# Kernel optimization log

Hardware: AMD Instinct MI355X
Metric: run time of the kernel (lower is better)

Reference implementation:

```python
import jax, jax.numpy as jnp
import numpy as np

N = 100000          # nodes
E = 1600000         # edges
NS_IN = 128         # input scalars (128x0e)
MUL_IN = 32         # input 1o multiplicity -> eq dim 96
NS_OUT = 64         # output scalars (64x0e)
MUL_OUT = 16        # output 1o multiplicity -> eq dim 48
HID = 256           # ScalarMLPFunction hidden width
WNUM = MUL_IN * MUL_OUT  # o3.Linear weight_numel (single l=1 path)


def setup_inputs() -> dict:
    key = jax.random.key(0)
    ks = jax.random.split(key, 6)
    return {
        "features": jax.random.normal(ks[0], (N, NS_IN + MUL_IN * 3), jnp.float32),
        "edge_index": jax.random.randint(ks[1], (2, E), 0, N, dtype=jnp.int32),
        "inv_W1": jax.random.normal(ks[2], (NS_IN, HID), jnp.float32),
        "inv_W2": jax.random.normal(ks[3], (HID, NS_OUT), jnp.float32),
        "wemb_W1": jax.random.normal(ks[4], (NS_IN, HID), jnp.float32),
        "wemb_W2": jax.random.normal(ks[5], (HID, WNUM), jnp.float32),
    }


def _mlp(x, W1, W2):
    # ScalarMLPFunction: fan-in-normalized linears with SiLU nonlinearity
    h = jax.nn.silu((x @ W1) * np.float32(1.0 / np.sqrt(W1.shape[0])))
    return (h @ W2) * np.float32(1.0 / np.sqrt(W2.shape[0]))


def reference(features, edge_index, inv_W1, inv_W2, wemb_W1, wemb_W2):
    # active_nodes = torch.unique(edge_index[0]); expressed jit-compatibly as a
    # boolean mask (out_features starts at zero; only active rows are written).
    active = jnp.zeros((N,), jnp.bool_).at[edge_index[0]].set(True)

    scalars = features[:, :NS_IN]                       # [N, 128]

    # invariant readout MLP -> first n_scalars_out channels
    inv_out = _mlp(scalars, inv_W1, inv_W2)             # [N, 64]

    # equivariant path: reshape_in -> [N, mul_in, 3]
    x_eq = features[:, NS_IN:].reshape(N, MUL_IN, 3)
    # per-node o3.Linear weights from weights_emb MLP
    w = _mlp(scalars, wemb_W1, wemb_W2).reshape(N, MUL_IN, MUL_OUT)
    # e3nn o3.Linear (shared_weights=False), single l=1 path, path-normalized
    eq_out = jnp.einsum('nim,nio->nom', x_eq, w) * np.float32(1.0 / np.sqrt(MUL_IN))
    eq_flat = eq_out.reshape(N, MUL_OUT * 3)            # inverse_reshape_irreps

    out = jnp.concatenate([inv_out, eq_flat], axis=-1)  # [N, 112]
    return out * active[:, None].astype(out.dtype)
```

## Files before the change

kernel.cpp:

```cpp
#include <hip/hip_runtime.h>

#define NN 100000
#define EE 1600000
#define FDIM 224
#define OUTC 112

#define SPO 0
#define HCG 16384
#define RNG 32768
#define XO  32768
#define WMO 65536
#define LDSZ 81920

typedef __attribute__((ext_vector_type(8))) short bf16x8;
typedef __attribute__((ext_vector_type(4))) float f32x4;
typedef __attribute__((ext_vector_type(4))) unsigned int u32x4;
typedef __attribute__((ext_vector_type(4))) int i32x4;

__device__ __forceinline__ unsigned short f2bf(float f) {
  unsigned u = __builtin_bit_cast(unsigned, f);
  u = (u + 0x7FFFu + ((u >> 16) & 1u)) >> 16;
  return (unsigned short)u;
}
__device__ __forceinline__ float bf2f(unsigned short h) {
  return __builtin_bit_cast(float, (unsigned)h << 16);
}
__device__ __forceinline__ unsigned cvtpk(float lo, float hi) {
  unsigned d;
  asm("v_cvt_pk_bf16_f32 %0, %1, %2" : "=v"(d) : "v"(lo), "v"(hi));
  return d;
}
__device__ __forceinline__ float fast_exp2(float t) {
  float e; asm("v_exp_f32 %0, %1" : "=v"(e) : "v"(t)); return e;
}
__device__ __forceinline__ float fast_rcp(float x) {
  float r; asm("v_rcp_f32 %0, %1" : "=v"(r) : "v"(x)); return r;
}
__device__ __forceinline__ float silu_rs(float a) {
  float v = a * 0.08838834764831845f;
  float e = fast_exp2(v * -1.442695041f);
  return v * fast_rcp(1.f + e);
}
__device__ __forceinline__ void gl_lds16(const unsigned short* g, char* l) {
  __builtin_amdgcn_global_load_lds(
      (const __attribute__((address_space(1))) unsigned int*)g,
      (__attribute__((address_space(3))) unsigned int*)l, 16, 0, 0);
}

#define WAITV(n) do { asm volatile("s_waitcnt vmcnt(" #n ")" ::: "memory"); \
                      __builtin_amdgcn_sched_barrier(0); } while (0)
#define WAITV_FOR(c) do { if ((c) <= 52) { WAITV(3); } else if ((c) == 53) { WAITV(2); } \
                          else if ((c) == 54) { WAITV(1); } else { WAITV(0); } } while (0)
#define LGKM0() asm volatile("s_waitcnt lgkmcnt(0)" ::: "memory")
#define LGKM_BAR() do { asm volatile("s_waitcnt lgkmcnt(0)" ::: "memory"); \
                        __builtin_amdgcn_s_barrier(); } while (0)
#define KEEP(x) asm volatile("" :: "v"(x))
#define MFMA(A, B, C) __builtin_amdgcn_mfma_f32_16x16x32_bf16((A), (B), (C), 0, 0, 0)
#define ISSUE(c) do { if ((c) < 56) \
    gl_lds16(Wall + (size_t)(c) * 4096 + wv * 512 + lane * 8, \
             smem + RNG + ((c) & 3) * 8192 + wv * 1024); } while (0)

__global__ void k_zero(unsigned int* p, int n) {
  int i = blockIdx.x * 256 + threadIdx.x;
  if (i < n) p[i] = 0u;
}

__global__ void k_scatter(const int* __restrict__ ei, unsigned char* __restrict__ act) {
  int e4 = blockIdx.x * 256 + threadIdx.x;
  if (e4 < EE / 4) {
    i32x4 v = *(const i32x4*)(ei + e4 * 4);
#pragma unroll
    for (int j = 0; j < 4; ++j) {
      int n = v[j];
      if (!act[n]) act[n] = 1;
    }
  }
}

__global__ void k_wprep(const float* __restrict__ invW1, const float* __restrict__ invW2,
                        const float* __restrict__ wembW1, const float* __restrict__ wembW2,
                        unsigned short* __restrict__ Wall) {
  int i = blockIdx.x * 256 + threadIdx.x;
  if (i >= 56 * 4096) return;
  int c = i >> 12, j = i & 4095;
  float v;
  if (c < 16) {
    int cg = c >> 3, sub = c & 7;
    if (sub < 4) {
      int r128 = j >> 5, slot = (j >> 3) & 3, e = j & 7;
      int gg = slot ^ (r128 & 3);
      int hc = cg * 128 + r128;
      int k = sub * 32 + gg * 8 + e;
      v = (hc < 256) ? invW1[k * 256 + hc] : wembW1[k * 256 + (hc - 256)];
    } else {
      int ks = sub - 4;
      int wseg = j >> 9, r16 = (j >> 5) & 15, slot = (j >> 3) & 3, e = j & 7;
      int gg = slot ^ (r16 & 3);
      int col = (wseg >> 1) * 16 + r16;
      int k = cg * 128 + ks * 32 + gg * 8 + e;
      v = invW2[k * 64 + col];
    }
  } else {
    int c2 = c - 16;
    int cgl = c2 / 20, sub = c2 % 20;
    int r128 = j >> 5, slot = (j >> 3) & 3, e = j & 7;
    int gg = slot ^ (r128 & 3);
    if (sub < 4) {
      int hc = (2 + cgl) * 128 + r128;
      int k = sub * 32 + gg * 8 + e;
      v = (hc < 256) ? invW1[k * 256 + hc] : wembW1[k * 256 + (hc - 256)];
    } else {
      int idx = sub - 4, ct = idx >> 2, ks = idx & 3;
      int col = ct * 128 + r128;
      int k = cgl * 128 + ks * 32 + gg * 8 + e;
      v = wembW2[k * 512 + col];
    }
  }
  Wall[i] = f2bf(v);
}

__global__ __launch_bounds__(512, 2) void k_main(
    const float* __restrict__ feats,
    const unsigned short* __restrict__ Wall,
    const unsigned char* __restrict__ act,
    float* __restrict__ out) {
  __shared__ char smem[LDSZ];
  const int tid = threadIdx.x;
  const int lane = tid & 63;
  const int wv = tid >> 6;
  const int o = lane & 15;
  const int g = lane >> 4;
  const int base = blockIdx.x * 64;

  const float inv16 = 0.0625f;
  const float rs32  = 0.17677669529663687f;

  const int srow = tid >> 3, sq = tid & 7;
  int gnode = base + srow; if (gnode > NN - 1) gnode = NN - 1;
  const float* sp = feats + (size_t)gnode * FDIM + sq * 16;
  f32x4 s0 = *(const f32x4*)sp;
  f32x4 s1 = *(const f32x4*)(sp + 4);
  f32x4 s2 = *(const f32x4*)(sp + 8);
  f32x4 s3 = *(const f32x4*)(sp + 12);
  const float* xp = feats + (size_t)gnode * FDIM + 128 + sq * 12;
  f32x4 x0 = *(const f32x4*)xp;
  f32x4 x1 = *(const f32x4*)(xp + 4);
  f32x4 x2 = *(const f32x4*)(xp + 8);

  {
    unsigned w0 = cvtpk(s0[0], s0[1]), w1 = cvtpk(s0[2], s0[3]);
    unsigned w2 = cvtpk(s1[0], s1[1]), w3 = cvtpk(s1[2], s1[3]);
    unsigned w4 = cvtpk(s2[0], s2[1]), w5 = cvtpk(s2[2], s2[3]);
    unsigned w6 = cvtpk(s3[0], s3[1]), w7 = cvtpk(s3[2], s3[3]);
    *(u32x4*)(smem + SPO + srow * 256 + (((sq * 2 + 0) ^ (srow & 15)) << 4)) =
        (u32x4){w0, w1, w2, w3};
    *(u32x4*)(smem + SPO + srow * 256 + (((sq * 2 + 1) ^ (srow & 15)) << 4)) =
        (u32x4){w4, w5, w6, w7};
  }
  unsigned xr[6];
  xr[0] = cvtpk(x0[0], x0[1]); xr[1] = cvtpk(x0[2], x0[3]);
  xr[2] = cvtpk(x1[0], x1[1]); xr[3] = cvtpk(x1[2], x1[3]);
  xr[4] = cvtpk(x2[0], x2[1]); xr[5] = cvtpk(x2[2], x2[3]);
#pragma unroll
  for (int j = 0; j < 6; ++j) KEEP(xr[j]);
  asm volatile("s_waitcnt vmcnt(0)" ::: "memory");
  LGKM_BAR();

  ISSUE(0); ISSUE(1); ISSUE(2); ISSUE(3);

  f32x4 accW[4][4], accA[4], acc2[2];
#pragma unroll
  for (int ct = 0; ct < 4; ++ct)
#pragma unroll
    for (int rt = 0; rt < 4; ++rt) accW[ct][rt] = (f32x4){0.f, 0.f, 0.f, 0.f};
#pragma unroll
  for (int rt = 0; rt < 4; ++rt) accA[rt] = (f32x4){0.f, 0.f, 0.f, 0.f};
  acc2[0] = (f32x4){0.f, 0.f, 0.f, 0.f};
  acc2[1] = (f32x4){0.f, 0.f, 0.f, 0.f};

#pragma unroll
  for (int cg = 0; cg < 4; ++cg) {
    const int cb = (cg < 2) ? cg * 8 : 16 + (cg - 2) * 20;
#pragma unroll
    for (int ks = 0; ks < 4; ++ks) {
      const int c = cb + ks;
      WAITV_FOR(c);
      __builtin_amdgcn_s_setprio(1);
      bf16x8 b = *(const bf16x8*)(smem + RNG + (c & 3) * 8192 +
                                  (wv * 16 + o) * 64 + ((g ^ (o & 3)) << 4));
#pragma unroll
      for (int rt = 0; rt < 4; ++rt) {
        bf16x8 a = *(const bf16x8*)(smem + SPO + (rt * 16 + o) * 256 +
                                    (((ks * 4 + g) ^ o) << 4));
        accA[rt] = MFMA(a, b, accA[rt]);
      }
      __builtin_amdgcn_s_setprio(0);
      LGKM0();
      ISSUE(c + 4);
    }
    {
      const int col = wv * 16 + o;
#pragma unroll
      for (int rt = 0; rt < 4; ++rt) {
#pragma unroll
        for (int rp = 0; rp < 2; ++rp) {
          unsigned w = cvtpk(silu_rs(accA[rt][rp * 2]), silu_rs(accA[rt][rp * 2 + 1]));
          int row0 = rt * 16 + g * 4 + rp * 2;
          *(unsigned short*)(smem + HCG + row0 * 256 +
                             ((col * 2) ^ ((row0 & 15) << 4))) = (unsigned short)w;
          int row1 = row0 + 1;
          *(unsigned short*)(smem + HCG + row1 * 256 +
                             ((col * 2) ^ ((row1 & 15) << 4))) = (unsigned short)(w >> 16);
        }
        accA[rt] = (f32x4){0.f, 0.f, 0.f, 0.f};
      }
    }
    LGKM_BAR();
    if (cg < 2) {
#pragma unroll
      for (int ks = 0; ks < 4; ++ks) {
        const int c = cb + 4 + ks;
        WAITV_FOR(c);
        __builtin_amdgcn_s_setprio(1);
        bf16x8 b = *(const bf16x8*)(smem + RNG + (c & 3) * 8192 + wv * 1024 +
                                    o * 64 + ((g ^ (o & 3)) << 4));
        const int rtl = wv & 1;
        bf16x8 a0 = *(const bf16x8*)(smem + HCG + (rtl * 16 + o) * 256 +
                                     (((ks * 4 + g) ^ o) << 4));
        bf16x8 a1 = *(const bf16x8*)(smem + HCG + ((rtl + 2) * 16 + o) * 256 +
                                     (((ks * 4 + g) ^ o) << 4));
        acc2[0] = MFMA(a0, b, acc2[0]);
        acc2[1] = MFMA(a1, b, acc2[1]);
        __builtin_amdgcn_s_setprio(0);
        LGKM0();
        ISSUE(c + 4);
      }
    } else {
#pragma unroll
      for (int ct = 0; ct < 4; ++ct)
#pragma unroll
        for (int ks = 0; ks < 4; ++ks) {
          const int c = cb + 4 + ct * 4 + ks;
          WAITV_FOR(c);
          __builtin_amdgcn_s_setprio(1);
          bf16x8 b = *(const bf16x8*)(smem + RNG + (c & 3) * 8192 +
                                      (wv * 16 + o) * 64 + ((g ^ (o & 3)) << 4));
#pragma unroll
          for (int rt = 0; rt < 4; ++rt) {
            bf16x8 a = *(const bf16x8*)(smem + HCG + (rt * 16 + o) * 256 +
                                        (((ks * 4 + g) ^ o) << 4));
            accW[ct][rt] = MFMA(a, b, accW[ct][rt]);
          }
          __builtin_amdgcn_s_setprio(0);
          LGKM0();
          ISSUE(c + 4);
        }
    }
    LGKM_BAR();
  }

  {
    const int xb = XO + srow * 192 + sq * 24;
#pragma unroll
    for (int j = 0; j < 6; ++j) *(unsigned*)(smem + xb + j * 4) = xr[j];
  }
  float eq[6] = {0.f, 0.f, 0.f, 0.f, 0.f, 0.f};
  const int nloc = tid >> 3, q = tid & 7;
#pragma unroll
  for (int Q = 0; Q < 4; ++Q) {
    const int lc = wv * 16 + o;
#pragma unroll
    for (int rt = 0; rt < 4; ++rt)
#pragma unroll
      for (int rp = 0; rp < 2; ++rp) {
        unsigned w = cvtpk(accW[Q][rt][rp * 2] * inv16, accW[Q][rt][rp * 2 + 1] * inv16);
        int n0 = rt * 16 + g * 4 + rp * 2;
        *(unsigned short*)(smem + WMO + n0 * 256 +
                           ((lc * 2) ^ ((n0 & 15) << 4))) = (unsigned short)w;
        int n1 = n0 + 1;
        *(unsigned short*)(smem + WMO + n1 * 256 +
                           ((lc * 2) ^ ((n1 & 15) << 4))) = (unsigned short)(w >> 16);
      }
    LGKM_BAR();
#pragma unroll
    for (int il = 0; il < 8; ++il) {
      unsigned wpair = *(const unsigned*)(smem + WMO + nloc * 256 +
                                          ((il * 32 + q * 4) ^ ((nloc & 15) << 4)));
      float wf0 = bf2f((unsigned short)wpair);
      float wf1 = bf2f((unsigned short)(wpair >> 16));
      const int xb = XO + nloc * 192 + (Q * 24 + il * 3) * 2;
#pragma unroll
      for (int m = 0; m < 3; ++m) {
        float xv = bf2f(*(const unsigned short*)(smem + xb + m * 2));
        eq[m] += xv * wf0;
        eq[3 + m] += xv * wf1;
      }
    }
    if (Q < 3) LGKM_BAR();
  }

#pragma unroll
  for (int jj = 0; jj < 2; ++jj) {
    const int rt = (wv & 1) + jj * 2;
#pragma unroll
    for (int r = 0; r < 4; ++r) {
      int node = base + rt * 16 + g * 4 + r;
      if (node < NN) {
        float s = act[node] ? inv16 : 0.f;
        out[(size_t)node * OUTC + (wv >> 1) * 16 + o] = acc2[jj][r] * s;
      }
    }
  }
  {
    int node = base + nloc;
    if (node < NN) {
      float sC = act[node] ? rs32 : 0.f;
      float* op = out + (size_t)node * OUTC + 64 + q * 6;
#pragma unroll
      for (int j = 0; j < 6; ++j) op[j] = eq[j] * sC;
    }
  }
}

extern "C" void kernel_launch(void* const* d_in, const int* in_sizes, int n_in,
                              void* d_out, int out_size, void* d_ws, size_t ws_size,
                              hipStream_t stream) {
  const float* feats = (const float*)d_in[0];
  const int* ei = (const int*)d_in[1];
  const float* invW1 = (const float*)d_in[2];
  const float* invW2 = (const float*)d_in[3];
  const float* wembW1 = (const float*)d_in[4];
  const float* wembW2 = (const float*)d_in[5];
  float* out = (float*)d_out;

  char* ws = (char*)d_ws;
  unsigned short* Wall = (unsigned short*)ws;
  unsigned char* act = (unsigned char*)(ws + 458752);

  k_zero<<<98, 256, 0, stream>>>((unsigned int*)act, 25024);
  k_scatter<<<1563, 256, 0, stream>>>(ei, act);
  k_wprep<<<896, 256, 0, stream>>>(invW1, invW2, wembW1, wembW2, Wall);
  k_main<<<1563, 512, 0, stream>>>(feats, Wall, act, out);
}
```

Measured before the change: 132.3 us.

## Halve node tile to 32 per block to cut LDS and raise occupancy

Each block now processes 32 nodes instead of 64. LDS use drops from 80KB to 48KB, the accumulator arrays shrink, and launch bounds ask for 4 blocks per CU instead of 2. Load, store and equivariant-contraction indexing are remapped to 16 threads per node, and the out-of-range bounds checks are removed because 100000 divides evenly by 32. The cost is that every block still streams the full weight set, so weight traffic per node doubles and each weight fetch feeds half as many MFMAs.

```diff
diff --git a/kernel.cpp b/kernel.cpp
--- a/kernel.cpp
+++ b/kernel.cpp
@@ -6,14 +6,15 @@
 #define OUTC 112
 
 #define SPO 0
-#define HCG 16384
-#define RNG 32768
-#define XO  32768
-#define WMO 65536
-#define LDSZ 81920
+#define HCG 8192
+#define RNG 16384
+#define XO  16384
+#define WMQ 24576
+#define LDSZ 49152
 
 typedef __attribute__((ext_vector_type(8))) short bf16x8;
 typedef __attribute__((ext_vector_type(4))) float f32x4;
+typedef __attribute__((ext_vector_type(2))) float f32x2;
 typedef __attribute__((ext_vector_type(4))) unsigned int u32x4;
 typedef __attribute__((ext_vector_type(4))) int i32x4;
 
@@ -119,7 +120,7 @@
   Wall[i] = f2bf(v);
 }
 
-__global__ __launch_bounds__(512, 2) void k_main(
+__global__ __launch_bounds__(512, 4) void k_main(
     const float* __restrict__ feats,
     const unsigned short* __restrict__ Wall,
     const unsigned char* __restrict__ act,
@@ -130,53 +131,45 @@
   const int wv = tid >> 6;
   const int o = lane & 15;
   const int g = lane >> 4;
-  const int base = blockIdx.x * 64;
+  const int base = blockIdx.x * 32;
 
   const float inv16 = 0.0625f;
   const float rs32  = 0.17677669529663687f;
 
-  const int srow = tid >> 3, sq = tid & 7;
-  int gnode = base + srow; if (gnode > NN - 1) gnode = NN - 1;
-  const float* sp = feats + (size_t)gnode * FDIM + sq * 16;
+  const int srow = tid >> 4, sq = tid & 15;
+  const float* sp = feats + (size_t)(base + srow) * FDIM + sq * 8;
   f32x4 s0 = *(const f32x4*)sp;
   f32x4 s1 = *(const f32x4*)(sp + 4);
-  f32x4 s2 = *(const f32x4*)(sp + 8);
-  f32x4 s3 = *(const f32x4*)(sp + 12);
-  const float* xp = feats + (size_t)gnode * FDIM + 128 + sq * 12;
-  f32x4 x0 = *(const f32x4*)xp;
-  f32x4 x1 = *(const f32x4*)(xp + 4);
-  f32x4 x2 = *(const f32x4*)(xp + 8);
+  const float* xp = feats + (size_t)(base + srow) * FDIM + 128 + sq * 6;
+  f32x2 xa = *(const f32x2*)xp;
+  f32x2 xb2 = *(const f32x2*)(xp + 2);
+  f32x2 xc = *(const f32x2*)(xp + 4);
 
   {
     unsigned w0 = cvtpk(s0[0], s0[1]), w1 = cvtpk(s0[2], s0[3]);
     unsigned w2 = cvtpk(s1[0], s1[1]), w3 = cvtpk(s1[2], s1[3]);
-    unsigned w4 = cvtpk(s2[0], s2[1]), w5 = cvtpk(s2[2], s2[3]);
-    unsigned w6 = cvtpk(s3[0], s3[1]), w7 = cvtpk(s3[2], s3[3]);
-    *(u32x4*)(smem + SPO + srow * 256 + (((sq * 2 + 0) ^ (srow & 15)) << 4)) =
+    *(u32x4*)(smem + SPO + srow * 256 + ((sq ^ (srow & 15)) << 4)) =
         (u32x4){w0, w1, w2, w3};
-    *(u32x4*)(smem + SPO + srow * 256 + (((sq * 2 + 1) ^ (srow & 15)) << 4)) =
-        (u32x4){w4, w5, w6, w7};
-  }
-  unsigned xr[6];
-  xr[0] = cvtpk(x0[0], x0[1]); xr[1] = cvtpk(x0[2], x0[3]);
-  xr[2] = cvtpk(x1[0], x1[1]); xr[3] = cvtpk(x1[2], x1[3]);
-  xr[4] = cvtpk(x2[0], x2[1]); xr[5] = cvtpk(x2[2], x2[3]);
-#pragma unroll
-  for (int j = 0; j < 6; ++j) KEEP(xr[j]);
+  }
+  unsigned xr[3];
+  xr[0] = cvtpk(xa[0], xa[1]);
+  xr[1] = cvtpk(xb2[0], xb2[1]);
+  xr[2] = cvtpk(xc[0], xc[1]);
+#pragma unroll
+  for (int j = 0; j < 3; ++j) KEEP(xr[j]);
   asm volatile("s_waitcnt vmcnt(0)" ::: "memory");
   LGKM_BAR();
 
   ISSUE(0); ISSUE(1); ISSUE(2); ISSUE(3);
 
-  f32x4 accW[4][4], accA[4], acc2[2];
+  f32x4 accW[4][2], accA[2], acc2;
 #pragma unroll
   for (int ct = 0; ct < 4; ++ct)
 #pragma unroll
-    for (int rt = 0; rt < 4; ++rt) accW[ct][rt] = (f32x4){0.f, 0.f, 0.f, 0.f};
-#pragma unroll
-  for (int rt = 0; rt < 4; ++rt) accA[rt] = (f32x4){0.f, 0.f, 0.f, 0.f};
-  acc2[0] = (f32x4){0.f, 0.f, 0.f, 0.f};
-  acc2[1] = (f32x4){0.f, 0.f, 0.f, 0.f};
+    for (int rt = 0; rt < 2; ++rt) accW[ct][rt] = (f32x4){0.f, 0.f, 0.f, 0.f};
+  accA[0] = (f32x4){0.f, 0.f, 0.f, 0.f};
+  accA[1] = (f32x4){0.f, 0.f, 0.f, 0.f};
+  acc2 = (f32x4){0.f, 0.f, 0.f, 0.f};
 
 #pragma unroll
   for (int cg = 0; cg < 4; ++cg) {
@@ -189,7 +182,7 @@
       bf16x8 b = *(const bf16x8*)(smem + RNG + (c & 3) * 8192 +
                                   (wv * 16 + o) * 64 + ((g ^ (o & 3)) << 4));
 #pragma unroll
-      for (int rt = 0; rt < 4; ++rt) {
+      for (int rt = 0; rt < 2; ++rt) {
         bf16x8 a = *(const bf16x8*)(smem + SPO + (rt * 16 + o) * 256 +
                                     (((ks * 4 + g) ^ o) << 4));
         accA[rt] = MFMA(a, b, accA[rt]);
@@ -201,7 +194,7 @@
     {
       const int col = wv * 16 + o;
 #pragma unroll
-      for (int rt = 0; rt < 4; ++rt) {
+      for (int rt = 0; rt < 2; ++rt) {
 #pragma unroll
         for (int rp = 0; rp < 2; ++rp) {
           unsigned w = cvtpk(silu_rs(accA[rt][rp * 2]), silu_rs(accA[rt][rp * 2 + 1]));
@@ -224,13 +217,9 @@
         __builtin_amdgcn_s_setprio(1);
         bf16x8 b = *(const bf16x8*)(smem + RNG + (c & 3) * 8192 + wv * 1024 +
                                     o * 64 + ((g ^ (o & 3)) << 4));
-        const int rtl = wv & 1;
-        bf16x8 a0 = *(const bf16x8*)(smem + HCG + (rtl * 16 + o) * 256 +
-                                     (((ks * 4 + g) ^ o) << 4));
-        bf16x8 a1 = *(const bf16x8*)(smem + HCG + ((rtl + 2) * 16 + o) * 256 +
-                                     (((ks * 4 + g) ^ o) << 4));
-        acc2[0] = MFMA(a0, b, acc2[0]);
-        acc2[1] = MFMA(a1, b, acc2[1]);
+        bf16x8 a = *(const bf16x8*)(smem + HCG + ((wv & 1) * 16 + o) * 256 +
+                                    (((ks * 4 + g) ^ o) << 4));
+        acc2 = MFMA(a, b, acc2);
         __builtin_amdgcn_s_setprio(0);
         LGKM0();
         ISSUE(c + 4);
@@ -246,7 +235,7 @@
           bf16x8 b = *(const bf16x8*)(smem + RNG + (c & 3) * 8192 +
                                       (wv * 16 + o) * 64 + ((g ^ (o & 3)) << 4));
 #pragma unroll
-          for (int rt = 0; rt < 4; ++rt) {
+          for (int rt = 0; rt < 2; ++rt) {
             bf16x8 a = *(const bf16x8*)(smem + HCG + (rt * 16 + o) * 256 +
                                         (((ks * 4 + g) ^ o) << 4));
             accW[ct][rt] = MFMA(a, b, accW[ct][rt]);
@@ -260,65 +249,55 @@
   }
 
   {
-    const int xb = XO + srow * 192 + sq * 24;
-#pragma unroll
-    for (int j = 0; j < 6; ++j) *(unsigned*)(smem + xb + j * 4) = xr[j];
-  }
-  float eq[6] = {0.f, 0.f, 0.f, 0.f, 0.f, 0.f};
-  const int nloc = tid >> 3, q = tid & 7;
+    const int xb = XO + srow * 192 + sq * 12;
+    *(unsigned*)(smem + xb + 0) = xr[0];
+    *(unsigned*)(smem + xb + 4) = xr[1];
+    *(unsigned*)(smem + xb + 8) = xr[2];
+  }
+  float eq[3] = {0.f, 0.f, 0.f};
+  const int nloc = tid >> 4, q = tid & 15;
 #pragma unroll
   for (int Q = 0; Q < 4; ++Q) {
     const int lc = wv * 16 + o;
 #pragma unroll
-    for (int rt = 0; rt < 4; ++rt)
+    for (int rt = 0; rt < 2; ++rt)
 #pragma unroll
       for (int rp = 0; rp < 2; ++rp) {
         unsigned w = cvtpk(accW[Q][rt][rp * 2] * inv16, accW[Q][rt][rp * 2 + 1] * inv16);
         int n0 = rt * 16 + g * 4 + rp * 2;
-        *(unsigned short*)(smem + WMO + n0 * 256 +
+        *(unsigned short*)(smem + WMQ + n0 * 256 +
                            ((lc * 2) ^ ((n0 & 15) << 4))) = (unsigned short)w;
         int n1 = n0 + 1;
-        *(unsigned short*)(smem + WMO + n1 * 256 +
+        *(unsigned short*)(smem + WMQ + n1 * 256 +
                            ((lc * 2) ^ ((n1 & 15) << 4))) = (unsigned short)(w >> 16);
       }
     LGKM_BAR();
 #pragma unroll
     for (int il = 0; il < 8; ++il) {
-      unsigned wpair = *(const unsigned*)(smem + WMO + nloc * 256 +
-                                          ((il * 32 + q * 4) ^ ((nloc & 15) << 4)));
-      float wf0 = bf2f((unsigned short)wpair);
-      float wf1 = bf2f((unsigned short)(wpair >> 16));
+      unsigned short w = *(const unsigned short*)(
+          smem + WMQ + nloc * 256 + (((il * 16 + q) * 2) ^ ((nloc & 15) << 4)));
+      float wf = bf2f(w);
       const int xb = XO + nloc * 192 + (Q * 24 + il * 3) * 2;
 #pragma unroll
-      for (int m = 0; m < 3; ++m) {
-        float xv = bf2f(*(const unsigned short*)(smem + xb + m * 2));
-        eq[m] += xv * wf0;
-        eq[3 + m] += xv * wf1;
-      }
+      for (int m = 0; m < 3; ++m)
+        eq[m] += bf2f(*(const unsigned short*)(smem + xb + m * 2)) * wf;
     }
     if (Q < 3) LGKM_BAR();
   }
 
 #pragma unroll
-  for (int jj = 0; jj < 2; ++jj) {
-    const int rt = (wv & 1) + jj * 2;
-#pragma unroll
-    for (int r = 0; r < 4; ++r) {
-      int node = base + rt * 16 + g * 4 + r;
-      if (node < NN) {
-        float s = act[node] ? inv16 : 0.f;
-        out[(size_t)node * OUTC + (wv >> 1) * 16 + o] = acc2[jj][r] * s;
-      }
-    }
+  for (int r = 0; r < 4; ++r) {
+    int node = base + (wv & 1) * 16 + g * 4 + r;
+    float s = act[node] ? inv16 : 0.f;
+    out[(size_t)node * OUTC + (wv >> 1) * 16 + o] = acc2[r] * s;
   }
   {
     int node = base + nloc;
-    if (node < NN) {
-      float sC = act[node] ? rs32 : 0.f;
-      float* op = out + (size_t)node * OUTC + 64 + q * 6;
-#pragma unroll
-      for (int j = 0; j < 6; ++j) op[j] = eq[j] * sC;
-    }
+    float sC = act[node] ? rs32 : 0.f;
+    float* op = out + (size_t)node * OUTC + 64 + q * 3;
+    op[0] = eq[0] * sC;
+    op[1] = eq[1] * sC;
+    op[2] = eq[2] * sC;
   }
 }
 
@@ -340,5 +319,5 @@
   k_zero<<<98, 256, 0, stream>>>((unsigned int*)act, 25024);
   k_scatter<<<1563, 256, 0, stream>>>(ei, act);
   k_wprep<<<896, 256, 0, stream>>>(invW1, invW2, wembW1, wembW2, Wall);
-  k_main<<<1563, 512, 0, stream>>>(feats, Wall, act, out);
-}
+  k_main<<<3125, 512, 0, stream>>>(feats, Wall, act, out);
+}
```

Result: faster. 116.6 us (-11.9%).
